# Performance work log

Measured on AMD Instinct MI355X. Metric: run time of the kernel, lower is better.

## Reference

```python
import jax, jax.numpy as jnp
import numpy as np

DIM, H, DH = 3072, 24, 128
MLP = int(DIM * 4.0)
EPS = 1e-6


def setup_inputs() -> dict:
    key = jax.random.key(0)
    ks = jax.random.split(key, 8)
    B, L = 2, 4096
    s = 0.02
    return {
        "hidden_states": jax.random.normal(ks[0], (B, L, DIM), jnp.float32),
        "temb": jax.random.normal(ks[1], (B, DIM), jnp.float32),
        "rope": jax.random.normal(ks[2], (L, DH // 2, 4), jnp.float32),
        "w_lin": jax.random.normal(ks[3], (DIM, 3 * DIM), jnp.float32) * s,
        "b_lin": jnp.zeros((3 * DIM,), jnp.float32),
        "w1": jax.random.normal(ks[4], (DIM, 3 * DIM + MLP), jnp.float32) * s,
        "b1": jnp.zeros((3 * DIM + MLP,), jnp.float32),
        "w2": jax.random.normal(ks[5], (DIM + MLP, DIM), jnp.float32) * s,
        "b2": jnp.zeros((DIM,), jnp.float32),
        "q_scale": jnp.ones((DH,), jnp.float32),
        "k_scale": jnp.ones((DH,), jnp.float32),
    }


def _rms(x, scale):
    return x * jax.lax.rsqrt(jnp.mean(x * x, axis=-1, keepdims=True) + EPS) * scale


def _rope(x, fr):
    # x: [B,H,L,DH]; fr: [L, DH//2, 2, 2]
    B, Hn, L, D = x.shape
    x_ = x.reshape(B, Hn, L, D // 2, 1, 2)
    out = fr[..., 0] * x_[..., 0] + fr[..., 1] * x_[..., 1]  # [B,H,L,D//2,2]
    return out.reshape(B, Hn, L, D)


def reference(hidden_states, temb, rope, w_lin, b_lin, w1, b1, w2, b2, q_scale, k_scale):
    B, L, _ = hidden_states.shape
    residual = hidden_states
    # AdaLayerNormZeroSingle
    emb = jax.nn.silu(temb) @ w_lin + b_lin  # [B, 3*DIM]
    shift, scale, gate = jnp.split(emb[:, None, :], 3, axis=-1)
    mu = jnp.mean(hidden_states, axis=-1, keepdims=True)
    var = jnp.mean(jnp.square(hidden_states - mu), axis=-1, keepdims=True)
    x = (hidden_states - mu) * jax.lax.rsqrt(var + EPS)
    x = x * (1 + scale) + shift
    # fused QKV + MLP projection
    proj = x @ w1 + b1
    qkv, mlp = proj[..., : 3 * DIM], proj[..., 3 * DIM :]
    qkv = qkv.reshape(B, L, 3, H, DH).transpose(2, 0, 3, 1, 4)  # [3,B,H,L,DH]
    q, k, v = qkv[0], qkv[1], qkv[2]
    q = _rms(q, q_scale)
    k = _rms(k, k_scale)
    fr = rope.reshape(L, DH // 2, 2, 2)
    q = _rope(q, fr)
    k = _rope(k, fr)
    # heads are MERGED before attention (faithful to source)
    q = q.transpose(0, 2, 1, 3).reshape(B, L, H * DH)
    k = k.transpose(0, 2, 1, 3).reshape(B, L, H * DH)
    v = v.transpose(0, 2, 1, 3).reshape(B, L, H * DH)
    attn = jax.nn.softmax(jnp.einsum("bqd,bkd->bqk", q, k) * (DH ** -0.5), axis=-1)
    attn_out = jnp.einsum("bqk,bkd->bqd", attn, v)
    h = jnp.concatenate([attn_out, jax.nn.gelu(mlp)], axis=-1) @ w2 + b2
    return residual + gate * h
```

## Files before the change

### kernel.cpp

```cpp
#include <hip/hip_runtime.h>
#include <hip/hip_fp16.h>

typedef _Float16 half_t;
typedef __attribute__((ext_vector_type(8))) _Float16 f16x8;
typedef __attribute__((ext_vector_type(4))) float f32x4;

#define DIM   3072
#define NH    24
#define DH    128
#define MLP_D 12288
#define LSEQ  4096
#define BATCH 2
#define NROWS 8192
#define N1    21504
#define QKV_N 9216
#define CAT_N 15360

__device__ __forceinline__ void gload16(const void* g, void* l) {
  __builtin_amdgcn_global_load_lds((const __attribute__((address_space(1))) void*)g,
                                   (__attribute__((address_space(3))) void*)l, 16, 0, 0);
}

__device__ __forceinline__ float gelu_tanh(float x) {
  float u = 0.7978845608028654f * (x + 0.044715f * x * x * x);
  float t = 1.f - 2.f / (__expf(2.f * u) + 1.f);
  return 0.5f * x * (1.f + t);
}

struct EpiParams {
  const float* bias;
  float* outF; int ldoF;
  half_t* o1; int ldo1;
  half_t* o2; int ldo2;
  const float* resid;
  const float* gate;
  float scale;
};

template<int EPI>
__global__ __launch_bounds__(512, 2) void gemm256(
    const half_t* __restrict__ A, int lda,
    const half_t* __restrict__ B, int ldb,
    int nbx, int nby, int nsplit, int K, EpiParams ep)
{
  __shared__ __align__(16) char lds[131072];
  const int t = threadIdx.x, lane = t & 63, wid = t >> 6;

  const int nwg = nbx * nby;
  const int wg = blockIdx.x;
  const int id = (wg & 7) * (nwg >> 3) + (wg >> 3);
  const int panel = 8 * nbx;
  const int bm = (id / panel) * 8 + (id % 8);
  const int bn = (id % panel) / 8;
  const int brow = bm * 256, bcol = bn * 256;
  const int wr = wid >> 2, wc = wid & 3;

  f32x4 acc[8][4];
#pragma unroll
  for (int m = 0; m < 8; ++m)
#pragma unroll
    for (int n = 0; n < 4; ++n) acc[m][n] = (f32x4){0.f, 0.f, 0.f, 0.f};

  const int scol = (((lane & 3) ^ ((lane >> 3) & 3)) * 8);
  const half_t* pA = A + (size_t)(brow + wid * 32 + (lane >> 2)) * lda + scol;
  const half_t* pB = B + (size_t)(bcol + wid * 32 + (lane >> 2)) * ldb + scol;
  const int wrow = wid * 2048;
  const int NT = K >> 6;

  const int pc = (((lane >> 4) ^ ((lane >> 1) & 3)) << 4);
  const int aoff = (wr * 128 + (lane & 15)) * 64 + pc;
  const int boff = 32768 + (wc * 64 + (lane & 15)) * 64 + pc;

  f16x8 bf[2][4];

#define STAGE_A(bb, kh, tk) {                                               \
    gload16(pA + (size_t)(tk) * 64 + (kh) * 32,                             \
            (bb) + (kh) * 16384 + wrow);                                    \
    gload16(pA + (size_t)(tk) * 64 + (kh) * 32 + (size_t)16 * lda,          \
            (bb) + (kh) * 16384 + wrow + 1024); }
#define STAGE_B(bb, kh, tk) {                                               \
    gload16(pB + (size_t)(tk) * 64 + (kh) * 32,                             \
            (bb) + 32768 + (kh) * 16384 + wrow);                            \
    gload16(pB + (size_t)(tk) * 64 + (kh) * 32 + (size_t)16 * ldb,          \
            (bb) + 32768 + (kh) * 16384 + wrow + 1024); }

  {
    char* b0 = lds;
    char* b1 = lds + 65536;
    STAGE_B(b0, 0, 0); STAGE_A(b0, 0, 0); STAGE_B(b0, 1, 0);
    STAGE_A(b0, 1, 0); STAGE_B(b1, 0, 1); STAGE_A(b1, 0, 1); STAGE_B(b1, 1, 1);
    asm volatile("s_waitcnt vmcnt(6)" ::: "memory");
    __builtin_amdgcn_s_barrier();
  }

#define PHASE_TAIL                                                          \
    __builtin_amdgcn_sched_barrier(0);                                      \
    __builtin_amdgcn_s_barrier();                                           \
    asm volatile("s_waitcnt lgkmcnt(0)" ::: "memory");                      \
    __builtin_amdgcn_sched_barrier(0);                                      \
    __builtin_amdgcn_s_setprio(1);

#define PHASE_END                                                           \
    __builtin_amdgcn_s_setprio(0);                                          \
    __builtin_amdgcn_sched_barrier(0);                                      \
    __builtin_amdgcn_s_barrier();

  for (int tt = 0; tt < NT; ++tt) {
    char* cb = lds + (size_t)(tt & 1) * 65536;
    char* nb = lds + (size_t)((tt & 1) ^ 1) * 65536;
    f16x8 af[4];

#pragma unroll
    for (int mi = 0; mi < 4; ++mi) af[mi] = *(const f16x8*)(cb + aoff + mi * 1024);
#pragma unroll
    for (int nj = 0; nj < 4; ++nj) bf[0][nj] = *(const f16x8*)(cb + boff + nj * 1024);
    if (tt + 1 < NT) STAGE_A(nb, 1, tt + 1);
    PHASE_TAIL
#pragma unroll
    for (int mi = 0; mi < 4; ++mi)
#pragma unroll
      for (int nj = 0; nj < 4; ++nj)
        acc[mi][nj] = __builtin_amdgcn_mfma_f32_16x16x32_f16(af[mi], bf[0][nj], acc[mi][nj], 0, 0, 0);
    PHASE_END

#pragma unroll
    for (int mi = 0; mi < 4; ++mi) af[mi] = *(const f16x8*)(cb + aoff + 4096 + mi * 1024);
#pragma unroll
    for (int nj = 0; nj < 4; ++nj) bf[1][nj] = *(const f16x8*)(cb + boff + 16384 + nj * 1024);
    if (tt + 2 < NT) STAGE_B(cb, 0, tt + 2);
    PHASE_TAIL
#pragma unroll
    for (int mi = 0; mi < 4; ++mi)
#pragma unroll
      for (int nj = 0; nj < 4; ++nj)
        acc[4 + mi][nj] = __builtin_amdgcn_mfma_f32_16x16x32_f16(af[mi], bf[0][nj], acc[4 + mi][nj], 0, 0, 0);
    PHASE_END

#pragma unroll
    for (int mi = 0; mi < 4; ++mi) af[mi] = *(const f16x8*)(cb + aoff + 16384 + mi * 1024);
    if (tt + 2 < NT) STAGE_A(cb, 0, tt + 2);
    PHASE_TAIL
#pragma unroll
    for (int mi = 0; mi < 4; ++mi)
#pragma unroll
      for (int nj = 0; nj < 4; ++nj)
        acc[mi][nj] = __builtin_amdgcn_mfma_f32_16x16x32_f16(af[mi], bf[1][nj], acc[mi][nj], 0, 0, 0);
    PHASE_END

#pragma unroll
    for (int mi = 0; mi < 4; ++mi) af[mi] = *(const f16x8*)(cb + aoff + 16384 + 4096 + mi * 1024);
    if (tt + 2 < NT) STAGE_B(cb, 1, tt + 2);
    PHASE_TAIL
#pragma unroll
    for (int mi = 0; mi < 4; ++mi)
#pragma unroll
      for (int nj = 0; nj < 4; ++nj)
        acc[4 + mi][nj] = __builtin_amdgcn_mfma_f32_16x16x32_f16(af[mi], bf[1][nj], acc[4 + mi][nj], 0, 0, 0);
    __builtin_amdgcn_s_setprio(0);
    __builtin_amdgcn_sched_barrier(0);
    if (tt + 2 < NT) asm volatile("s_waitcnt vmcnt(6)" ::: "memory");
    else             asm volatile("s_waitcnt vmcnt(0)" ::: "memory");
    __builtin_amdgcn_s_barrier();
  }
#undef STAGE_A
#undef STAGE_B
#undef PHASE_TAIL
#undef PHASE_END

  const int laneR = lane & 15;
  const int colb = bcol + wc * 64;
  const int rowb = brow + wr * 128 + (lane >> 4) * 4;
#pragma unroll
  for (int mi = 0; mi < 8; ++mi) {
#pragma unroll
    for (int nj = 0; nj < 4; ++nj) {
      int col = colb + nj * 16 + laneR;
#pragma unroll
      for (int j = 0; j < 4; ++j) {
        int row = rowb + mi * 16 + j;
        float v = acc[mi][nj][j];
        if (EPI == 0) {
          v += ep.bias[col];
          if (col < nsplit) {
            ep.o1[(size_t)row * ep.ldo1 + col] = (half_t)v;
          } else {
            ep.o2[(size_t)row * ep.ldo2 + DIM + (col - nsplit)] = (half_t)gelu_tanh(v);
          }
        } else if (EPI == 1) {
          ep.outF[(size_t)row * ep.ldoF + col] = v * ep.scale;
        } else if (EPI == 2) {
          ep.o2[(size_t)row * ep.ldo2 + col] = (half_t)v;
        } else {
          v += ep.bias[col];
          int b = row >> 12;
          float g = ep.gate[(size_t)b * QKV_N + col];
          float r = ep.resid[(size_t)row * DIM + col];
          ep.outF[(size_t)row * ep.ldoF + col] = r + g * v;
        }
      }
    }
  }
}

__global__ __launch_bounds__(256) void k_emb(
    const float* __restrict__ temb, const float* __restrict__ w_lin,
    const float* __restrict__ b_lin, float* __restrict__ emb)
{
  __shared__ float s[DIM];
  int b = blockIdx.y;
  int col = blockIdx.x * 256 + threadIdx.x;
  const float* tr = temb + (size_t)b * DIM;
  for (int k = threadIdx.x; k < DIM; k += 256) {
    float x = tr[k];
    s[k] = x / (1.f + __expf(-x));
  }
  __syncthreads();
  float acc = b_lin[col];
  for (int k = 0; k < DIM; k += 4) {
    acc += s[k] * w_lin[(size_t)k * QKV_N + col]
         + s[k + 1] * w_lin[(size_t)(k + 1) * QKV_N + col]
         + s[k + 2] * w_lin[(size_t)(k + 2) * QKV_N + col]
         + s[k + 3] * w_lin[(size_t)(k + 3) * QKV_N + col];
  }
  emb[(size_t)b * QKV_N + col] = acc;
}

__global__ __launch_bounds__(256) void k_lnmod(
    const float* __restrict__ hs, const float* __restrict__ emb,
    half_t* __restrict__ xmod)
{
  int row = blockIdx.x;
  int b = row >> 12;
  const float* x = hs + (size_t)row * DIM;
  int t = threadIdx.x;
  float s = 0.f, s2 = 0.f;
  float4 v[3];
#pragma unroll
  for (int i = 0; i < 3; ++i) {
    v[i] = ((const float4*)x)[t + 256 * i];
    s  += v[i].x + v[i].y + v[i].z + v[i].w;
    s2 += v[i].x * v[i].x + v[i].y * v[i].y + v[i].z * v[i].z + v[i].w * v[i].w;
  }
  for (int o = 32; o; o >>= 1) { s += __shfl_xor(s, o); s2 += __shfl_xor(s2, o); }
  __shared__ float rs[4], rs2[4];
  int lane = t & 63, w = t >> 6;
  if (lane == 0) { rs[w] = s; rs2[w] = s2; }
  __syncthreads();
  s = rs[0] + rs[1] + rs[2] + rs[3];
  s2 = rs2[0] + rs2[1] + rs2[2] + rs2[3];
  float mu = s * (1.f / DIM);
  float var = s2 * (1.f / DIM) - mu * mu;
  float rstd = rsqrtf(var + 1e-6f);
  const float* shift = emb + (size_t)b * QKV_N;
  const float* scale = shift + DIM;
#pragma unroll
  for (int i = 0; i < 3; ++i) {
    int g = t + 256 * i;
    float4 sc = ((const float4*)scale)[g];
    float4 sh = ((const float4*)shift)[g];
    half_t ob[4];
    float vv[4] = {v[i].x, v[i].y, v[i].z, v[i].w};
    float scv[4] = {sc.x, sc.y, sc.z, sc.w};
    float shv[4] = {sh.x, sh.y, sh.z, sh.w};
#pragma unroll
    for (int j = 0; j < 4; ++j) {
      float xn = (vv[j] - mu) * rstd;
      ob[j] = (half_t)(xn * (1.f + scv[j]) + shv[j]);
    }
    *(uint2*)&xmod[(size_t)row * DIM + g * 4] = *(uint2*)ob;
  }
}

__global__ __launch_bounds__(256) void k_transpose_cvt(
    const float* __restrict__ in, half_t* __restrict__ out, int R, int C)
{
  __shared__ float s[64][65];
  int c0 = blockIdx.x * 64, r0 = blockIdx.y * 64;
  int tx = threadIdx.x & 63, ty = threadIdx.x >> 6;
#pragma unroll
  for (int j = 0; j < 16; ++j) {
    int r = ty + j * 4;
    s[r][tx] = in[(size_t)(r0 + r) * C + c0 + tx];
  }
  __syncthreads();
#pragma unroll
  for (int j = 0; j < 16; ++j) {
    int c = ty + j * 4;
    out[(size_t)(c0 + c) * R + r0 + tx] = (half_t)s[tx][c];
  }
}

__global__ __launch_bounds__(256) void k_qk_rmsrope(
    half_t* __restrict__ qkv, const float* __restrict__ rope,
    const float* __restrict__ q_scale, const float* __restrict__ k_scale)
{
  int w = blockIdx.x * 4 + (threadIdx.x >> 6);
  int lane = threadIdx.x & 63;
  int qk = w & 1;
  int hr = w >> 1;
  int h = hr % 24;
  int bl = hr / 24;
  size_t base = (size_t)bl * QKV_N + qk * DIM + h * DH;
  float x0 = (float)qkv[base + lane * 2];
  float x1 = (float)qkv[base + lane * 2 + 1];
  float ss = x0 * x0 + x1 * x1;
  for (int o = 32; o; o >>= 1) ss += __shfl_xor(ss, o);
  float r = rsqrtf(ss * (1.f / DH) + 1e-6f);
  const float* sc = qk ? k_scale : q_scale;
  float xs0 = x0 * r * sc[lane * 2];
  float xs1 = x1 * r * sc[lane * 2 + 1];
  int l = bl & (LSEQ - 1);
  float4 fr = ((const float4*)rope)[(size_t)l * 64 + lane];
  qkv[base + lane * 2]     = (half_t)(fr.x * xs0 + fr.y * xs1);
  qkv[base + lane * 2 + 1] = (half_t)(fr.z * xs0 + fr.w * xs1);
}

__global__ __launch_bounds__(256) void k_vT(
    const half_t* __restrict__ qkv, half_t* __restrict__ vT)
{
  __shared__ half_t s[64][65];
  int b = blockIdx.z;
  int l0 = blockIdx.x * 64, d0 = blockIdx.y * 64;
  int tx = threadIdx.x & 63, ty = threadIdx.x >> 6;
#pragma unroll
  for (int j = 0; j < 16; ++j) {
    int l = ty + j * 4;
    s[l][tx] = qkv[(size_t)(b * LSEQ + l0 + l) * QKV_N + 2 * DIM + d0 + tx];
  }
  __syncthreads();
#pragma unroll
  for (int j = 0; j < 16; ++j) {
    int d = ty + j * 4;
    vT[((size_t)b * DIM + d0 + d) * LSEQ + l0 + tx] = s[tx][d];
  }
}

__global__ __launch_bounds__(256) void k_softmax(
    const float* __restrict__ S, half_t* __restrict__ P)
{
  int row = blockIdx.x;
  const float* srow = S + (size_t)row * LSEQ;
  int t = threadIdx.x;
  float4 v[4];
  float mx = -1e30f;
#pragma unroll
  for (int i = 0; i < 4; ++i) {
    v[i] = ((const float4*)srow)[t + 256 * i];
    mx = fmaxf(mx, fmaxf(fmaxf(v[i].x, v[i].y), fmaxf(v[i].z, v[i].w)));
  }
  for (int o = 32; o; o >>= 1) mx = fmaxf(mx, __shfl_xor(mx, o));
  __shared__ float rmx[4], rsum[4];
  int lane = t & 63, w = t >> 6;
  if (lane == 0) rmx[w] = mx;
  __syncthreads();
  mx = fmaxf(fmaxf(rmx[0], rmx[1]), fmaxf(rmx[2], rmx[3]));
  float s = 0.f;
#pragma unroll
  for (int i = 0; i < 4; ++i) {
    v[i].x = __expf(v[i].x - mx); v[i].y = __expf(v[i].y - mx);
    v[i].z = __expf(v[i].z - mx); v[i].w = __expf(v[i].w - mx);
    s += v[i].x + v[i].y + v[i].z + v[i].w;
  }
  for (int o = 32; o; o >>= 1) s += __shfl_xor(s, o);
  if (lane == 0) rsum[w] = s;
  __syncthreads();
  s = rsum[0] + rsum[1] + rsum[2] + rsum[3];
  float inv = 1.f / s;
#pragma unroll
  for (int i = 0; i < 4; ++i) {
    half_t ob[4] = {
      (half_t)(v[i].x * inv), (half_t)(v[i].y * inv),
      (half_t)(v[i].z * inv), (half_t)(v[i].w * inv)};
    *(uint2*)&P[(size_t)row * LSEQ + (t + 256 * i) * 4] = *(uint2*)ob;
  }
}

extern "C" void kernel_launch(void* const* d_in, const int* in_sizes, int n_in,
                              void* d_out, int out_size, void* d_ws, size_t ws_size,
                              hipStream_t stream) {
  const float* hs      = (const float*)d_in[0];
  const float* temb    = (const float*)d_in[1];
  const float* rope    = (const float*)d_in[2];
  const float* w_lin   = (const float*)d_in[3];
  const float* b_lin   = (const float*)d_in[4];
  const float* w1      = (const float*)d_in[5];
  const float* b1      = (const float*)d_in[6];
  const float* w2      = (const float*)d_in[7];
  const float* b2      = (const float*)d_in[8];
  const float* q_scale = (const float*)d_in[9];
  const float* k_scale = (const float*)d_in[10];
  float* out = (float*)d_out;

  char* ws = (char*)d_ws;
  size_t off = 0;
  auto alloc = [&](size_t bytes) { char* p = ws + off; off += (bytes + 255) & ~(size_t)255; return p; };
  float*  emb    = (float*) alloc((size_t)BATCH * QKV_N * 4);
  half_t* xmod   = (half_t*)alloc((size_t)NROWS * DIM * 2);
  half_t* w1T    = (half_t*)alloc((size_t)N1 * DIM * 2);
  half_t* w2T    = (half_t*)alloc((size_t)DIM * CAT_N * 2);
  half_t* qkv    = (half_t*)alloc((size_t)NROWS * QKV_N * 2);
  half_t* concat = (half_t*)alloc((size_t)NROWS * CAT_N * 2);
  half_t* vT     = (half_t*)alloc((size_t)BATCH * DIM * LSEQ * 2);
  float*  Sbuf   = (float*) alloc((size_t)LSEQ * LSEQ * 4);
  half_t* Pbuf   = (half_t*)alloc((size_t)LSEQ * LSEQ * 2);
  (void)ws_size; (void)n_in; (void)in_sizes; (void)out_size;

  k_emb<<<dim3(QKV_N / 256, BATCH), 256, 0, stream>>>(temb, w_lin, b_lin, emb);
  k_transpose_cvt<<<dim3(N1 / 64, DIM / 64), 256, 0, stream>>>(w1, w1T, DIM, N1);
  k_transpose_cvt<<<dim3(DIM / 64, CAT_N / 64), 256, 0, stream>>>(w2, w2T, CAT_N, DIM);
  k_lnmod<<<NROWS, 256, 0, stream>>>(hs, emb, xmod);

  EpiParams ep1 = {b1, nullptr, 0, qkv, QKV_N, concat, CAT_N, nullptr, nullptr, 0.f};
  gemm256<0><<<(N1 / 256) * (NROWS / 256), 512, 0, stream>>>(
      xmod, DIM, w1T, DIM, N1 / 256, NROWS / 256, QKV_N, DIM, ep1);

  k_qk_rmsrope<<<(NROWS * NH * 2) / 4, 256, 0, stream>>>(qkv, rope, q_scale, k_scale);
  k_vT<<<dim3(LSEQ / 64, DIM / 64, BATCH), 256, 0, stream>>>(qkv, vT);

  for (int b = 0; b < BATCH; ++b) {
    const half_t* qb = qkv + (size_t)b * LSEQ * QKV_N;
    EpiParams epS = {nullptr, Sbuf, LSEQ, nullptr, 0, nullptr, 0, nullptr, nullptr, 0.08838834764831845f};
    gemm256<1><<<(LSEQ / 256) * (LSEQ / 256), 512, 0, stream>>>(
        qb, QKV_N, qb + DIM, QKV_N, LSEQ / 256, LSEQ / 256, 0, DIM, epS);
    k_softmax<<<LSEQ, 256, 0, stream>>>(Sbuf, Pbuf);
    EpiParams epPV = {nullptr, nullptr, 0, nullptr, 0,
                      concat + (size_t)b * LSEQ * CAT_N, CAT_N, nullptr, nullptr, 0.f};
    gemm256<2><<<(DIM / 256) * (LSEQ / 256), 512, 0, stream>>>(
        Pbuf, LSEQ, vT + (size_t)b * DIM * LSEQ, LSEQ, DIM / 256, LSEQ / 256, 0, LSEQ, epPV);
  }

  EpiParams ep2 = {b2, out, DIM, nullptr, 0, nullptr, 0, hs, emb + 2 * DIM, 0.f};
  gemm256<3><<<(DIM / 256) * (NROWS / 256), 512, 0, stream>>>(
      concat, CAT_N, w2T, CAT_N, DIM / 256, NROWS / 256, 0, CAT_N, ep2);
}
```

Before: 2.930 ms.

## Double-buffer A/B fragment registers to prefetch LDS reads before MFMA phases

Restructures the GEMM main loop so the LDS fragment loads for the next quarter-step go into a second register buffer while the current MFMAs run. This cuts one barrier per phase and lets ds_reads overlap MFMA work. The prologue now stages all tiles for the first two k-steps and preloads the first fragments. The price is more VGPRs from the doubled af array and a reordered global-load schedule whose vmcnt accounting must stay correct.

Result: faster. 2.817 ms (-3.9%).

```diff
diff --git a/kernel.cpp b/kernel.cpp
--- a/kernel.cpp
+++ b/kernel.cpp
@@ -71,7 +71,7 @@
   const int aoff = (wr * 128 + (lane & 15)) * 64 + pc;
   const int boff = 32768 + (wc * 64 + (lane & 15)) * 64 + pc;
 
-  f16x8 bf[2][4];
+  f16x8 af[2][4], bf[2][4];
 
 #define STAGE_A(bb, kh, tk) {                                               \
     gload16(pA + (size_t)(tk) * 64 + (kh) * 32,                             \
@@ -84,88 +84,91 @@
     gload16(pB + (size_t)(tk) * 64 + (kh) * 32 + (size_t)16 * ldb,          \
             (bb) + 32768 + (kh) * 16384 + wrow + 1024); }
 
+#define MFMA_Q(accoff, ab, bb2)                                             \
+    _Pragma("unroll")                                                       \
+    for (int mi = 0; mi < 4; ++mi)                                          \
+      _Pragma("unroll")                                                     \
+      for (int nj = 0; nj < 4; ++nj)                                        \
+        acc[(accoff) + mi][nj] = __builtin_amdgcn_mfma_f32_16x16x32_f16(    \
+            af[ab][mi], bf[bb2][nj], acc[(accoff) + mi][nj], 0, 0, 0);
+
+#define PHASE_HEAD                                                          \
+    asm volatile("s_waitcnt lgkmcnt(0)" ::: "memory");                      \
+    __builtin_amdgcn_sched_barrier(0);                                      \
+    __builtin_amdgcn_s_setprio(1);
+
+#define PHASE_MID                                                           \
+    __builtin_amdgcn_s_setprio(0);                                          \
+    __builtin_amdgcn_sched_barrier(0);
+
   {
     char* b0 = lds;
     char* b1 = lds + 65536;
-    STAGE_B(b0, 0, 0); STAGE_A(b0, 0, 0); STAGE_B(b0, 1, 0);
-    STAGE_A(b0, 1, 0); STAGE_B(b1, 0, 1); STAGE_A(b1, 0, 1); STAGE_B(b1, 1, 1);
-    asm volatile("s_waitcnt vmcnt(6)" ::: "memory");
-    __builtin_amdgcn_s_barrier();
-  }
-
-#define PHASE_TAIL                                                          \
-    __builtin_amdgcn_sched_barrier(0);                                      \
-    __builtin_amdgcn_s_barrier();                                           \
-    asm volatile("s_waitcnt lgkmcnt(0)" ::: "memory");                      \
-    __builtin_amdgcn_sched_barrier(0);                                      \
-    __builtin_amdgcn_s_setprio(1);
-
-#define PHASE_END                                                           \
-    __builtin_amdgcn_s_setprio(0);                                          \
-    __builtin_amdgcn_sched_barrier(0);                                      \
-    __builtin_amdgcn_s_barrier();
+    STAGE_B(b0, 0, 0); STAGE_A(b0, 0, 0); STAGE_B(b0, 1, 0); STAGE_A(b0, 1, 0);
+    STAGE_B(b1, 0, 1); STAGE_A(b1, 0, 1); STAGE_B(b1, 1, 1); STAGE_A(b1, 1, 1);
+    asm volatile("s_waitcnt vmcnt(8)" ::: "memory");
+    __builtin_amdgcn_s_barrier();
+#pragma unroll
+    for (int mi = 0; mi < 4; ++mi) af[0][mi] = *(const f16x8*)(lds + aoff + mi * 1024);
+#pragma unroll
+    for (int nj = 0; nj < 4; ++nj) bf[0][nj] = *(const f16x8*)(lds + boff + nj * 1024);
+    __builtin_amdgcn_sched_barrier(0);
+    __builtin_amdgcn_s_barrier();
+  }
 
   for (int tt = 0; tt < NT; ++tt) {
     char* cb = lds + (size_t)(tt & 1) * 65536;
     char* nb = lds + (size_t)((tt & 1) ^ 1) * 65536;
-    f16x8 af[4];
-
-#pragma unroll
-    for (int mi = 0; mi < 4; ++mi) af[mi] = *(const f16x8*)(cb + aoff + mi * 1024);
-#pragma unroll
-    for (int nj = 0; nj < 4; ++nj) bf[0][nj] = *(const f16x8*)(cb + boff + nj * 1024);
-    if (tt + 1 < NT) STAGE_A(nb, 1, tt + 1);
-    PHASE_TAIL
-#pragma unroll
-    for (int mi = 0; mi < 4; ++mi)
-#pragma unroll
-      for (int nj = 0; nj < 4; ++nj)
-        acc[mi][nj] = __builtin_amdgcn_mfma_f32_16x16x32_f16(af[mi], bf[0][nj], acc[mi][nj], 0, 0, 0);
-    PHASE_END
-
-#pragma unroll
-    for (int mi = 0; mi < 4; ++mi) af[mi] = *(const f16x8*)(cb + aoff + 4096 + mi * 1024);
+
+    PHASE_HEAD
+    MFMA_Q(0, 0, 0)
+    PHASE_MID
+#pragma unroll
+    for (int mi = 0; mi < 4; ++mi) af[1][mi] = *(const f16x8*)(cb + aoff + 4096 + mi * 1024);
+    if (tt + 2 < NT) STAGE_B(cb, 0, tt + 2);
+    __builtin_amdgcn_sched_barrier(0);
+    __builtin_amdgcn_s_barrier();
+
+    PHASE_HEAD
+    MFMA_Q(4, 1, 0)
+    PHASE_MID
+#pragma unroll
+    for (int mi = 0; mi < 4; ++mi) af[0][mi] = *(const f16x8*)(cb + aoff + 16384 + mi * 1024);
 #pragma unroll
     for (int nj = 0; nj < 4; ++nj) bf[1][nj] = *(const f16x8*)(cb + boff + 16384 + nj * 1024);
-    if (tt + 2 < NT) STAGE_B(cb, 0, tt + 2);
-    PHASE_TAIL
-#pragma unroll
-    for (int mi = 0; mi < 4; ++mi)
-#pragma unroll
-      for (int nj = 0; nj < 4; ++nj)
-        acc[4 + mi][nj] = __builtin_amdgcn_mfma_f32_16x16x32_f16(af[mi], bf[0][nj], acc[4 + mi][nj], 0, 0, 0);
-    PHASE_END
-
-#pragma unroll
-    for (int mi = 0; mi < 4; ++mi) af[mi] = *(const f16x8*)(cb + aoff + 16384 + mi * 1024);
     if (tt + 2 < NT) STAGE_A(cb, 0, tt + 2);
-    PHASE_TAIL
-#pragma unroll
-    for (int mi = 0; mi < 4; ++mi)
-#pragma unroll
-      for (int nj = 0; nj < 4; ++nj)
-        acc[mi][nj] = __builtin_amdgcn_mfma_f32_16x16x32_f16(af[mi], bf[1][nj], acc[mi][nj], 0, 0, 0);
-    PHASE_END
-
-#pragma unroll
-    for (int mi = 0; mi < 4; ++mi) af[mi] = *(const f16x8*)(cb + aoff + 16384 + 4096 + mi * 1024);
+    __builtin_amdgcn_sched_barrier(0);
+    __builtin_amdgcn_s_barrier();
+
+    PHASE_HEAD
+    MFMA_Q(0, 0, 1)
+    PHASE_MID
+#pragma unroll
+    for (int mi = 0; mi < 4; ++mi) af[1][mi] = *(const f16x8*)(cb + aoff + 16384 + 4096 + mi * 1024);
     if (tt + 2 < NT) STAGE_B(cb, 1, tt + 2);
-    PHASE_TAIL
-#pragma unroll
-    for (int mi = 0; mi < 4; ++mi)
-#pragma unroll
-      for (int nj = 0; nj < 4; ++nj)
-        acc[4 + mi][nj] = __builtin_amdgcn_mfma_f32_16x16x32_f16(af[mi], bf[1][nj], acc[4 + mi][nj], 0, 0, 0);
-    __builtin_amdgcn_s_setprio(0);
     __builtin_amdgcn_sched_barrier(0);
     if (tt + 2 < NT) asm volatile("s_waitcnt vmcnt(6)" ::: "memory");
     else             asm volatile("s_waitcnt vmcnt(0)" ::: "memory");
     __builtin_amdgcn_s_barrier();
+
+    PHASE_HEAD
+    MFMA_Q(4, 1, 1)
+    PHASE_MID
+    if (tt + 1 < NT) {
+#pragma unroll
+      for (int mi = 0; mi < 4; ++mi) af[0][mi] = *(const f16x8*)(nb + aoff + mi * 1024);
+#pragma unroll
+      for (int nj = 0; nj < 4; ++nj) bf[0][nj] = *(const f16x8*)(nb + boff + nj * 1024);
+    }
+    if (tt + 2 < NT) STAGE_A(cb, 1, tt + 2);
+    __builtin_amdgcn_sched_barrier(0);
+    __builtin_amdgcn_s_barrier();
   }
 #undef STAGE_A
 #undef STAGE_B
-#undef PHASE_TAIL
-#undef PHASE_END
+#undef MFMA_Q
+#undef PHASE_HEAD
+#undef PHASE_MID
 
   const int laneR = lane & 15;
   const int colb = bcol + wc * 64;
```
